# Optimization experiments

Measured on AMD Instinct MI355X. Metric: run time of the kernel, lower is better.

Reference implementation:

```python
import jax, jax.numpy as jnp
import numpy as np

BETA = 0.25
N_CODES = 1024
CODE_DIM = 64


def setup_inputs() -> dict:
    key = jax.random.key(0)
    k1, k2 = jax.random.split(key)
    z_e = jax.random.normal(k1, (32, CODE_DIM, 2048), dtype=jnp.float32)
    # nn.init.uniform_(weight, -1/n_codes, 1/n_codes)
    lim = 1.0 / N_CODES
    codebook = jax.random.uniform(k2, (N_CODES, CODE_DIM), dtype=jnp.float32,
                                  minval=-lim, maxval=lim)
    return {"z_e": z_e, "codebook": codebook}


def reference(z_e, codebook):
    B, C, K = z_e.shape
    # (B, C, K) -> (B*K, C)
    z = jnp.transpose(z_e, (0, 2, 1)).reshape(-1, C)
    # squared L2 distances: ||z||^2 + ||e||^2 - 2 z.e  -> (N, n_codes)
    dist = (jnp.sum(z * z, axis=1, keepdims=True)
            + jnp.sum(codebook * codebook, axis=1)[None, :]
            - 2.0 * (z @ codebook.T))
    codes = jnp.argmin(dist, axis=1)  # (N,)
    # gather quantized vectors, back to (B, C, K)
    z_q = jnp.transpose(codebook[codes].reshape(B, K, C), (0, 2, 1))
    # straight-through
    z_q_st = z_e + jax.lax.stop_gradient(z_q - z_e)
    sg = jax.lax.stop_gradient
    loss_codebook = jnp.mean((z_q - sg(z_e)) ** 2)
    loss_commit = jnp.mean((z_e - sg(z_q)) ** 2)
    loss_vq = loss_codebook + BETA * loss_commit
    # perplexity via histogram (equivalent to onehot.mean(0))
    n = codes.shape[0]
    avg_probs = jnp.zeros((N_CODES,), dtype=jnp.float32).at[codes].add(1.0) / n
    perplexity = jnp.exp(-jnp.sum(avg_probs * jnp.log(avg_probs + 1e-10)))
    return z_q_st, codes.reshape(B, K), loss_vq, perplexity
```

## Files before the change

### kernel.cpp

```cpp
#include <hip/hip_runtime.h>
#include <math.h>

#define NB 32
#define NC 64
#define NK 2048
#define NCODES 1024
#define NVEC (NB*NK)
#define NELEM (NB*NC*NK)
#define NBLK (NVEC/64)

#define MARGIN 1.5e-3f
#define CAP 32

#define WS_HIST  0
#define WS_CBN32 4096
#define WS_PART  8192
#define WS_CBBF  32768

typedef __bf16 bf16x8 __attribute__((ext_vector_type(8)));
typedef float  f32x4  __attribute__((ext_vector_type(4)));
#define MFMA16(A, B, ACC) __builtin_amdgcn_mfma_f32_16x16x32_bf16(A, B, ACC, 0, 0, 0)

__global__ void k_cbprep(const float* __restrict__ cb, float* __restrict__ n32,
                         __bf16* __restrict__ cbbf, int* __restrict__ hist) {
    const int t = threadIdx.x;
    const int j = blockIdx.x * 64 + t;
    if (blockIdx.x == 0) {
        int4 z4; z4.x = 0; z4.y = 0; z4.z = 0; z4.w = 0;
#pragma unroll
        for (int i = 0; i < 4; i++) ((int4*)hist)[t * 4 + i] = z4;
    }
    const float* cr = cb + (size_t)j * NC;
    float x[64];
#pragma unroll
    for (int i = 0; i < 16; i++) {
        f32x4 tv = *(const f32x4*)(cr + 4 * i);
        x[4*i+0] = tv[0]; x[4*i+1] = tv[1]; x[4*i+2] = tv[2]; x[4*i+3] = tv[3];
    }
    float r[8];
#pragma unroll
    for (int q = 0; q < 8; q++) r[q] = __fmul_rn(x[q], x[q]);
#pragma unroll
    for (int i = 8; i < 64; i += 8)
#pragma unroll
        for (int q = 0; q < 8; q++)
            r[q] = __fadd_rn(r[q], __fmul_rn(x[i + q], x[i + q]));
    float s01 = __fadd_rn(r[0], r[1]), s23 = __fadd_rn(r[2], r[3]);
    float s45 = __fadd_rn(r[4], r[5]), s67 = __fadd_rn(r[6], r[7]);
    n32[j] = __fadd_rn(__fadd_rn(s01, s23), __fadd_rn(s45, s67));
    __bf16* br = cbbf + (size_t)j * NC;
#pragma unroll
    for (int i = 0; i < 8; i++) {
        bf16x8 o;
#pragma unroll
        for (int q = 0; q < 8; q++) o[q] = (__bf16)x[8*i + q];
        *(bf16x8*)(br + 8*i) = o;
    }
}

__launch_bounds__(512, 2)
__global__ void k_vq(const float* __restrict__ ze, const float* __restrict__ cb,
                     const float* __restrict__ n32, const __bf16* __restrict__ cbbf,
                     int* __restrict__ hist, float* __restrict__ codes_f,
                     float* __restrict__ outq, double* __restrict__ part) {
    __shared__ float wmin[64][8];
    __shared__ float gthr[64];
    __shared__ int cnt[64];
    __shared__ int cand[64][CAP];
    __shared__ unsigned long long keys2[64][8];
    __shared__ int codearr[64];
    __shared__ double lsd[8];

    const int t = threadIdx.x;
    const int L = t & 63;
    const int w = t >> 6;
    const int quad = L >> 4;
    const int col = L & 15;
    const int vec0 = blockIdx.x * 64;
    const int b = vec0 >> 11;
    const int k0 = vec0 & (NK - 1);
    const float* zbase = ze + (size_t)b * NC * NK + k0;

    bf16x8 bfr[8][2];
    float n32v[8];
#pragma unroll
    for (int tile = 0; tile < 8; tile++) {
        const __bf16* brow = cbbf + (size_t)(w*128 + tile*16 + col) * NC + quad*8;
        bfr[tile][0] = *(const bf16x8*)(brow);
        bfr[tile][1] = *(const bf16x8*)(brow + 32);
        n32v[tile] = n32[w*128 + tile*16 + col];
    }
    bf16x8 af[4][2];
#pragma unroll
    for (int vt = 0; vt < 4; vt++)
#pragma unroll
        for (int kt = 0; kt < 2; kt++)
#pragma unroll
            for (int j = 0; j < 8; j++)
                af[vt][kt][j] =
                    (__bf16)zbase[(size_t)(kt*32 + quad*8 + j) * NK + vt*16 + col];

    float pmin[4][4];
#pragma unroll
    for (int vt = 0; vt < 4; vt++)
#pragma unroll
        for (int r = 0; r < 4; r++) pmin[vt][r] = 1e30f;
#pragma unroll
    for (int tile = 0; tile < 8; tile++) {
#pragma unroll
        for (int vt = 0; vt < 4; vt++) {
            f32x4 acc = {0.f, 0.f, 0.f, 0.f};
            acc = MFMA16(af[vt][0], bfr[tile][0], acc);
            acc = MFMA16(af[vt][1], bfr[tile][1], acc);
#pragma unroll
            for (int r = 0; r < 4; r++) {
                float pd = __fsub_rn(n32v[tile], __fmul_rn(2.f, acc[r]));
                pmin[vt][r] = fminf(pmin[vt][r], pd);
            }
        }
    }
#pragma unroll
    for (int vt = 0; vt < 4; vt++)
#pragma unroll
        for (int r = 0; r < 4; r++) {
            float pm = pmin[vt][r];
            pm = fminf(pm, __shfl_xor(pm, 1, 16));
            pm = fminf(pm, __shfl_xor(pm, 2, 16));
            pm = fminf(pm, __shfl_xor(pm, 4, 16));
            pm = fminf(pm, __shfl_xor(pm, 8, 16));
            if (col == 0) wmin[vt*16 + quad*4 + r][w] = pm;
        }
    __syncthreads();

    if (t < 64) {
        float g = wmin[t][0];
#pragma unroll
        for (int ww = 1; ww < 8; ww++) g = fminf(g, wmin[t][ww]);
        gthr[t] = g + MARGIN;
        cnt[t] = 0;
    }
    __syncthreads();

    float thr[4][4];
#pragma unroll
    for (int vt = 0; vt < 4; vt++)
#pragma unroll
        for (int r = 0; r < 4; r++) thr[vt][r] = gthr[vt*16 + quad*4 + r];
#pragma unroll
    for (int tile = 0; tile < 8; tile++) {
#pragma unroll
        for (int vt = 0; vt < 4; vt++) {
            f32x4 acc = {0.f, 0.f, 0.f, 0.f};
            acc = MFMA16(af[vt][0], bfr[tile][0], acc);
            acc = MFMA16(af[vt][1], bfr[tile][1], acc);
#pragma unroll
            for (int r = 0; r < 4; r++) {
                float pd = __fsub_rn(n32v[tile], __fmul_rn(2.f, acc[r]));
                if (pd <= thr[vt][r]) {
                    int m = vt*16 + quad*4 + r;
                    int slot = atomicAdd(&cnt[m], 1);
                    if (slot < CAP) cand[m][slot] = w*128 + tile*16 + col;
                }
            }
        }
    }
    __syncthreads();

    {
        const int v = L;
        float rr[8];
#pragma unroll
        for (int q = 0; q < 8; q++) {
            float xx = zbase[(size_t)q * NK + v];
            rr[q] = __fmul_rn(xx, xx);
        }
#pragma unroll
        for (int i = 8; i < 64; i += 8)
#pragma unroll
            for (int q = 0; q < 8; q++) {
                float xx = zbase[(size_t)(i + q) * NK + v];
                rr[q] = __fadd_rn(rr[q], __fmul_rn(xx, xx));
            }
        float s01 = __fadd_rn(rr[0], rr[1]), s23 = __fadd_rn(rr[2], rr[3]);
        float s45 = __fadd_rn(rr[4], rr[5]), s67 = __fadd_rn(rr[6], rr[7]);
        float t1 = __fadd_rn(__fadd_rn(s01, s23), __fadd_rn(s45, s67));

        int cc = cnt[v];
        unsigned long long kmin = 0xFFFFFFFFFFFFFFFFULL;
        if (cc <= CAP) {
            for (int si = w; si < cc; si += 8) {
                int j = cand[v][si];
                const float* cr = cb + (size_t)j * NC;
                float a = 0.f;
#pragma unroll
                for (int c = 0; c < NC; c++)
                    a = __fmaf_rn(zbase[(size_t)c * NK + v], cr[c], a);
                float d = __fsub_rn(__fadd_rn(t1, n32[j]), __fmul_rn(2.f, a));
                unsigned long long key =
                    ((unsigned long long)__float_as_uint(d) << 32) | (unsigned int)j;
                if (key < kmin) kmin = key;
            }
        } else {
            for (int j = w * 128; j < (w + 1) * 128; j++) {
                const float* cr = cb + (size_t)j * NC;
                float a = 0.f;
#pragma unroll
                for (int c = 0; c < NC; c++)
                    a = __fmaf_rn(zbase[(size_t)c * NK + v], cr[c], a);
                float d = __fsub_rn(__fadd_rn(t1, n32[j]), __fmul_rn(2.f, a));
                unsigned long long key =
                    ((unsigned long long)__float_as_uint(d) << 32) | (unsigned int)j;
                if (key < kmin) kmin = key;
            }
        }
        keys2[v][w] = kmin;
    }
    __syncthreads();

    if (t < 64) {
        unsigned long long kmin = keys2[t][0];
#pragma unroll
        for (int ww = 1; ww < 8; ww++) {
            unsigned long long kk = keys2[t][ww];
            if (kk < kmin) kmin = kk;
        }
        int code = (int)(kmin & 0xFFFFFFFFu);
        codearr[t] = code;
        codes_f[vec0 + t] = (float)code;
        atomicAdd(&hist[code], 1);
    }
    __syncthreads();

    double s = 0.0;
    float* ob = outq + (size_t)b * NC * NK + k0;
    const int c0 = t >> 4;
    const int v0 = (t & 15) * 4;
    int cds[4];
#pragma unroll
    for (int u = 0; u < 4; u++) cds[u] = codearr[v0 + u];
#pragma unroll
    for (int half = 0; half < 2; half++) {
        const int c = c0 + half * 32;
        f32x4 zv = *(const f32x4*)(zbase + (size_t)c * NK + v0);
        f32x4 ov;
#pragma unroll
        for (int u = 0; u < 4; u++) {
            float qv = cb[(size_t)cds[u] * NC + c];
            ov[u] = __fadd_rn(zv[u], __fsub_rn(qv, zv[u]));
            double d = (double)qv - (double)zv[u];
            s += d * d;
        }
        *(f32x4*)(ob + (size_t)c * NK + v0) = ov;
    }
    for (int off = 32; off; off >>= 1) s += __shfl_down(s, off);
    if (L == 0) lsd[w] = s;
    __syncthreads();
    if (t == 0) {
        double tot = 0.0;
#pragma unroll
        for (int i = 0; i < 8; i++) tot += lsd[i];
        part[blockIdx.x] = tot;
    }
}

__launch_bounds__(1024)
__global__ void k_final(const double* __restrict__ part, const int* __restrict__ hist,
                        float* __restrict__ out) {
    int t = threadIdx.x;
    double vL = part[t];
    double p = (double)hist[t] * (1.0 / (double)NVEC);
    double vE = p * log(p + 1e-10);
    for (int off = 32; off; off >>= 1) {
        vL += __shfl_down(vL, off);
        vE += __shfl_down(vE, off);
    }
    __shared__ double lsL[16], lsE[16];
    int lane = t & 63, wv = t >> 6;
    if (lane == 0) { lsL[wv] = vL; lsE[wv] = vE; }
    __syncthreads();
    if (t == 0) {
        double SL = 0.0, SE = 0.0;
        for (int i = 0; i < 16; i++) { SL += lsL[i]; SE += lsE[i]; }
        double loss_cb = SL / (double)NELEM;
        out[NELEM + NVEC]     = (float)(loss_cb + 0.25 * loss_cb);
        out[NELEM + NVEC + 1] = (float)exp(-SE);
    }
}

extern "C" void kernel_launch(void* const* d_in, const int* in_sizes, int n_in,
                              void* d_out, int out_size, void* d_ws, size_t ws_size,
                              hipStream_t stream) {
    const float* ze = (const float*)d_in[0];
    const float* cb = (const float*)d_in[1];
    float* out = (float*)d_out;
    char* ws = (char*)d_ws;

    int*    hist = (int*)(ws + WS_HIST);
    float*  n32  = (float*)(ws + WS_CBN32);
    double* part = (double*)(ws + WS_PART);
    __bf16* cbbf = (__bf16*)(ws + WS_CBBF);

    float* zq      = out;
    float* codes_f = out + NELEM;

    k_cbprep<<<16, 64, 0, stream>>>(cb, n32, cbbf, hist);
    k_vq<<<NBLK, 512, 0, stream>>>(ze, cb, n32, cbbf, hist, codes_f, zq, part);
    k_final<<<1, 1024, 0, stream>>>(part, hist, out);
}
```

Baseline: 152.9 us.

## Halve VQ block to four waves, streaming codebook fragments per tile

The VQ kernel now runs 256 threads (4 waves) per 64-vector block, so each wave covers 256 codes instead of 128. The codebook bf16 fragments and norms, previously held in registers across both passes, are now loaded inside each tile iteration, which frees registers. Launch bounds move to 256x4 so more blocks can be resident. In exchange the codebook is read twice per block from cache/global memory, and per-wave serial work (tiles, exact rescoring, fallback scan) doubles.

```diff
diff --git a/kernel.cpp b/kernel.cpp
--- a/kernel.cpp
+++ b/kernel.cpp
@@ -58,18 +58,18 @@
     }
 }
 
-__launch_bounds__(512, 2)
+__launch_bounds__(256, 4)
 __global__ void k_vq(const float* __restrict__ ze, const float* __restrict__ cb,
                      const float* __restrict__ n32, const __bf16* __restrict__ cbbf,
                      int* __restrict__ hist, float* __restrict__ codes_f,
                      float* __restrict__ outq, double* __restrict__ part) {
-    __shared__ float wmin[64][8];
+    __shared__ float wmin[64][4];
     __shared__ float gthr[64];
     __shared__ int cnt[64];
     __shared__ int cand[64][CAP];
-    __shared__ unsigned long long keys2[64][8];
+    __shared__ unsigned long long keys2[64][4];
     __shared__ int codearr[64];
-    __shared__ double lsd[8];
+    __shared__ double lsd[4];
 
     const int t = threadIdx.x;
     const int L = t & 63;
@@ -81,15 +81,6 @@
     const int k0 = vec0 & (NK - 1);
     const float* zbase = ze + (size_t)b * NC * NK + k0;
 
-    bf16x8 bfr[8][2];
-    float n32v[8];
-#pragma unroll
-    for (int tile = 0; tile < 8; tile++) {
-        const __bf16* brow = cbbf + (size_t)(w*128 + tile*16 + col) * NC + quad*8;
-        bfr[tile][0] = *(const bf16x8*)(brow);
-        bfr[tile][1] = *(const bf16x8*)(brow + 32);
-        n32v[tile] = n32[w*128 + tile*16 + col];
-    }
     bf16x8 af[4][2];
 #pragma unroll
     for (int vt = 0; vt < 4; vt++)
@@ -105,16 +96,20 @@
     for (int vt = 0; vt < 4; vt++)
 #pragma unroll
         for (int r = 0; r < 4; r++) pmin[vt][r] = 1e30f;
-#pragma unroll
-    for (int tile = 0; tile < 8; tile++) {
+#pragma unroll 4
+    for (int tile = 0; tile < 16; tile++) {
+        const __bf16* brow = cbbf + (size_t)(w*256 + tile*16 + col) * NC + quad*8;
+        bf16x8 b0 = *(const bf16x8*)(brow);
+        bf16x8 b1 = *(const bf16x8*)(brow + 32);
+        float nvv = n32[w*256 + tile*16 + col];
 #pragma unroll
         for (int vt = 0; vt < 4; vt++) {
             f32x4 acc = {0.f, 0.f, 0.f, 0.f};
-            acc = MFMA16(af[vt][0], bfr[tile][0], acc);
-            acc = MFMA16(af[vt][1], bfr[tile][1], acc);
+            acc = MFMA16(af[vt][0], b0, acc);
+            acc = MFMA16(af[vt][1], b1, acc);
 #pragma unroll
             for (int r = 0; r < 4; r++) {
-                float pd = __fsub_rn(n32v[tile], __fmul_rn(2.f, acc[r]));
+                float pd = __fsub_rn(nvv, __fmul_rn(2.f, acc[r]));
                 pmin[vt][r] = fminf(pmin[vt][r], pd);
             }
         }
@@ -135,7 +130,7 @@
     if (t < 64) {
         float g = wmin[t][0];
 #pragma unroll
-        for (int ww = 1; ww < 8; ww++) g = fminf(g, wmin[t][ww]);
+        for (int ww = 1; ww < 4; ww++) g = fminf(g, wmin[t][ww]);
         gthr[t] = g + MARGIN;
         cnt[t] = 0;
     }
@@ -146,20 +141,24 @@
     for (int vt = 0; vt < 4; vt++)
 #pragma unroll
         for (int r = 0; r < 4; r++) thr[vt][r] = gthr[vt*16 + quad*4 + r];
-#pragma unroll
-    for (int tile = 0; tile < 8; tile++) {
+#pragma unroll 4
+    for (int tile = 0; tile < 16; tile++) {
+        const __bf16* brow = cbbf + (size_t)(w*256 + tile*16 + col) * NC + quad*8;
+        bf16x8 b0 = *(const bf16x8*)(brow);
+        bf16x8 b1 = *(const bf16x8*)(brow + 32);
+        float nvv = n32[w*256 + tile*16 + col];
 #pragma unroll
         for (int vt = 0; vt < 4; vt++) {
             f32x4 acc = {0.f, 0.f, 0.f, 0.f};
-            acc = MFMA16(af[vt][0], bfr[tile][0], acc);
-            acc = MFMA16(af[vt][1], bfr[tile][1], acc);
+            acc = MFMA16(af[vt][0], b0, acc);
+            acc = MFMA16(af[vt][1], b1, acc);
 #pragma unroll
             for (int r = 0; r < 4; r++) {
-                float pd = __fsub_rn(n32v[tile], __fmul_rn(2.f, acc[r]));
+                float pd = __fsub_rn(nvv, __fmul_rn(2.f, acc[r]));
                 if (pd <= thr[vt][r]) {
                     int m = vt*16 + quad*4 + r;
                     int slot = atomicAdd(&cnt[m], 1);
-                    if (slot < CAP) cand[m][slot] = w*128 + tile*16 + col;
+                    if (slot < CAP) cand[m][slot] = w*256 + tile*16 + col;
                 }
             }
         }
@@ -188,7 +187,7 @@
         int cc = cnt[v];
         unsigned long long kmin = 0xFFFFFFFFFFFFFFFFULL;
         if (cc <= CAP) {
-            for (int si = w; si < cc; si += 8) {
+            for (int si = w; si < cc; si += 4) {
                 int j = cand[v][si];
                 const float* cr = cb + (size_t)j * NC;
                 float a = 0.f;
@@ -201,7 +200,7 @@
                 if (key < kmin) kmin = key;
             }
         } else {
-            for (int j = w * 128; j < (w + 1) * 128; j++) {
+            for (int j = w * 256; j < (w + 1) * 256; j++) {
                 const float* cr = cb + (size_t)j * NC;
                 float a = 0.f;
 #pragma unroll
@@ -220,7 +219,7 @@
     if (t < 64) {
         unsigned long long kmin = keys2[t][0];
 #pragma unroll
-        for (int ww = 1; ww < 8; ww++) {
+        for (int ww = 1; ww < 4; ww++) {
             unsigned long long kk = keys2[t][ww];
             if (kk < kmin) kmin = kk;
         }
@@ -239,8 +238,8 @@
 #pragma unroll
     for (int u = 0; u < 4; u++) cds[u] = codearr[v0 + u];
 #pragma unroll
-    for (int half = 0; half < 2; half++) {
-        const int c = c0 + half * 32;
+    for (int half = 0; half < 4; half++) {
+        const int c = c0 + half * 16;
         f32x4 zv = *(const f32x4*)(zbase + (size_t)c * NK + v0);
         f32x4 ov;
 #pragma unroll
@@ -258,7 +257,7 @@
     if (t == 0) {
         double tot = 0.0;
 #pragma unroll
-        for (int i = 0; i < 8; i++) tot += lsd[i];
+        for (int i = 0; i < 4; i++) tot += lsd[i];
         part[blockIdx.x] = tot;
     }
 }
@@ -304,6 +303,6 @@
     float* codes_f = out + NELEM;
 
     k_cbprep<<<16, 64, 0, stream>>>(cb, n32, cbbf, hist);
-    k_vq<<<NBLK, 512, 0, stream>>>(ze, cb, n32, cbbf, hist, codes_f, zq, part);
+    k_vq<<<NBLK, 256, 0, stream>>>(ze, cb, n32, cbbf, hist, codes_f, zq, part);
     k_final<<<1, 1024, 0, stream>>>(part, hist, out);
 }
```

Result: faster. 128.4 us (-16.0%).
